# Performance work log

Measured on AMD Instinct MI355X. Metric: run time of the kernel, lower is better.

The kernel has to match this reference:

```python
import jax, jax.numpy as jnp
import numpy as np

NUM_TYPES = 8
NUM_TAGS = 1 + 2 * NUM_TYPES  # tag 0 = 'O', 2t+1 = 'B-t', 2t+2 = 'I-t'
NEG = -10000.0


def _bio_constraints(num_types):
    K = 1 + 2 * num_types
    allowed = np.zeros((K, K), dtype=np.float32)
    for i in range(K):
        for j in range(K):
            if j == 0 or (j % 2 == 1):  # to O or to B-y: always allowed
                allowed[i, j] = 1.0
            else:  # to I-y: only from B-y or I-y
                y = (j - 2) // 2
                if i in (2 * y + 1, 2 * y + 2):
                    allowed[i, j] = 1.0
    start = np.array([1.0 if (j == 0 or j % 2 == 1) else 0.0 for j in range(K)], dtype=np.float32)
    end = np.ones((K,), dtype=np.float32)  # BIO: any tag may end a sequence
    return allowed, start, end


def setup_inputs() -> dict:
    key = jax.random.key(0)
    ks = jax.random.split(key, 8)
    B, T, D, K = 64, 512, 1024, NUM_TAGS
    mlm_out = jax.random.normal(ks[0], (B, T, D), dtype=jnp.float32)
    lengths = jax.random.randint(ks[1], (B,), T // 4, T + 1)  # variable lengths >= 1
    mask = (jnp.arange(T)[None, :] < lengths[:, None])  # bool [B,T], left-padded-free
    gold = jax.random.randint(ks[2], (B, T), 0, K)
    W = jax.random.normal(ks[3], (D, K), dtype=jnp.float32) * 0.02
    b = jnp.zeros((K,), dtype=jnp.float32)
    transitions = jax.random.normal(ks[4], (K, K), dtype=jnp.float32) * 0.1
    start_trans = jax.random.normal(ks[5], (K,), dtype=jnp.float32) * 0.1
    end_trans = jax.random.normal(ks[6], (K,), dtype=jnp.float32) * 0.1
    ta, sa, ea = _bio_constraints(NUM_TYPES)
    return {"mlm_out": mlm_out, "mask": mask, "gold": gold, "W": W, "b": b,
            "transitions": transitions, "start_trans": start_trans, "end_trans": end_trans,
            "trans_allowed": jnp.asarray(ta), "start_allowed": jnp.asarray(sa), "end_allowed": jnp.asarray(ea)}


def reference(mlm_out, mask, gold, W, b, transitions, start_trans, end_trans,
              trans_allowed, start_allowed, end_allowed):
    logits = jnp.einsum('btd,dk->btk', mlm_out, W) + b  # [B,T,K]
    maskf = mask.astype(logits.dtype)
    B, T, K = logits.shape

    # ---- joint (numerator) score, AllenNLP semantics ----
    score = start_trans[gold[:, 0]]
    pair = transitions[gold[:, :-1], gold[:, 1:]]                       # [B,T-1]
    emit = jnp.take_along_axis(logits, gold[:, :, None], axis=2)[..., 0]  # [B,T]
    score = score + jnp.sum(pair * maskf[:, 1:], axis=1) + jnp.sum(emit[:, :-1] * maskf[:, :-1], axis=1)
    lengths = jnp.sum(mask.astype(jnp.int32), axis=1)
    last_tags = jnp.take_along_axis(gold, (lengths - 1)[:, None], axis=1)[:, 0]
    last_emit = jnp.take_along_axis(logits[:, -1, :], last_tags[:, None], axis=1)[:, 0]
    score = score + end_trans[last_tags] + last_emit * maskf[:, -1]

    # ---- partition function (forward algorithm, log-space scan over time) ----
    logits_t = jnp.swapaxes(logits, 0, 1)  # [T,B,K]
    mask_t = jnp.swapaxes(maskf, 0, 1)     # [T,B]
    alpha0 = start_trans + logits_t[0]

    def fstep(alpha, xs):
        emit_t, m = xs
        inner = alpha[:, :, None] + transitions[None] + emit_t[:, None, :]  # [B,K,K]
        new = jax.scipy.special.logsumexp(inner, axis=1)
        return jnp.where(m[:, None] > 0, new, alpha), None

    alphaT, _ = jax.lax.scan(fstep, alpha0, (logits_t[1:], mask_t[1:]))
    logZ = jax.scipy.special.logsumexp(alphaT + end_trans, axis=1)

    loss = -jnp.sum(score - logZ)  # loss_weight = 1.0

    # ---- Viterbi decode with BIO-constrained transitions ----
    ct = transitions * trans_allowed + NEG * (1.0 - trans_allowed)
    cs = start_trans * start_allowed + NEG * (1.0 - start_allowed)
    ce = end_trans * end_allowed + NEG * (1.0 - end_allowed)
    v0 = cs + logits_t[0]

    def vstep(v, xs):
        emit_t, m = xs
        inner = v[:, :, None] + ct[None]          # [B,K,K]
        bp = jnp.argmax(inner, axis=1)            # [B,K] best prev tag per next tag
        best = jnp.max(inner, axis=1) + emit_t
        return jnp.where(m[:, None] > 0, best, v), bp

    vT, bps = jax.lax.scan(vstep, v0, (logits_t[1:], mask_t[1:]))  # bps [T-1,B,K]
    last_tag = jnp.argmax(vT + ce, axis=1)  # [B]

    def btstep(tag, xs):
        bp, m = xs
        prev = jnp.take_along_axis(bp, tag[:, None], axis=1)[:, 0]
        prev = jnp.where(m > 0, prev, tag)  # padded steps: carry tag through
        return prev, tag

    first_tag, tags_rest = jax.lax.scan(btstep, last_tag, (bps, mask_t[1:]), reverse=True)
    pred = jnp.concatenate([first_tag[None], tags_rest], axis=0).swapaxes(0, 1)  # [B,T]
    pred = pred * mask.astype(pred.dtype)
    return logits, loss, pred
```

## Files before the change

### kernel.cpp

```cpp
#include <hip/hip_runtime.h>
#include <math.h>

#define KK 17
#define TT 512
#define DD 1024
#define NBATCH 64
#define NEGC -10000.0f
#define NINF -1e30f

__device__ __forceinline__ float wsum64(float v) {
#pragma unroll
  for (int s = 32; s >= 1; s >>= 1) v += __shfl_xor(v, s);
  return v;
}
__device__ __forceinline__ int wsum64i(int v) {
#pragma unroll
  for (int s = 32; s >= 1; s >>= 1) v += __shfl_xor(v, s);
  return v;
}
__device__ __forceinline__ float rl(float x, int i) {
  return __int_as_float(__builtin_amdgcn_readlane(__float_as_int(x), i));
}

__global__ __launch_bounds__(512) void k_logits(const float* __restrict__ X,
                                                const float* __restrict__ W,
                                                const float* __restrict__ b,
                                                float* __restrict__ logits) {
  __shared__ float Ws[512 * KK];
  const int tid = threadIdx.x;
  const int lane = tid & 63;
  const int wv = tid >> 6;
  const long r0 = (long)blockIdx.x * 16 + wv * 2;
  const float* x0 = X + r0 * DD;
  float a0[KK], a1[KK];
#pragma unroll
  for (int j = 0; j < KK; ++j) { a0[j] = 0.f; a1[j] = 0.f; }

  for (int half = 0; half < 2; ++half) {
    __syncthreads();
#pragma unroll
    for (int i = 0; i < KK; ++i) {
      int idx = tid + i * 512;
      Ws[idx] = W[half * 512 * KK + idx];
    }
    __syncthreads();
#pragma unroll
    for (int it = 0; it < 8; ++it) {
      int k = it * 64 + lane;
      float xa = x0[half * 512 + k];
      float xb = x0[DD + half * 512 + k];
#pragma unroll
      for (int j = 0; j < KK; ++j) {
        float w = Ws[k * KK + j];
        a0[j] = fmaf(xa, w, a0[j]);
        a1[j] = fmaf(xb, w, a1[j]);
      }
    }
  }
#pragma unroll
  for (int j = 0; j < KK; ++j) { a0[j] = wsum64(a0[j]); a1[j] = wsum64(a1[j]); }
  if (lane < KK) {
    float v0 = 0.f, v1 = 0.f;
#pragma unroll
    for (int j = 0; j < KK; ++j)
      if (lane == j) { v0 = a0[j]; v1 = a1[j]; }
    float bb = b[lane];
    logits[r0 * KK + lane] = v0 + bb;
    logits[(r0 + 1) * KK + lane] = v1 + bb;
  }
}

#define ARGM(vl, il, vr, ir, vo, io) \
  { bool tk = (vr) > (vl); vo = tk ? (vr) : (vl); io = tk ? (ir) : (il); }

__global__ __launch_bounds__(256) void k_scan(
    const float* __restrict__ logits, const void* __restrict__ maskp,
    const int* __restrict__ gold, const float* __restrict__ trans,
    const float* __restrict__ st, const float* __restrict__ et,
    const float* __restrict__ ta, const float* __restrict__ sa,
    const float* __restrict__ ea, float* __restrict__ lossp,
    float* __restrict__ predp) {
  __shared__ __align__(16) float EM[513 * KK];
  __shared__ __align__(4) unsigned char Mk[512];
  __shared__ unsigned char BPt[511 * KK];
  __shared__ unsigned char G2t[256 * KK];
  __shared__ unsigned char G4t[128 * KK];
  __shared__ unsigned char G8t[64 * KK];
  __shared__ unsigned char PR[512];
  __shared__ float red[2];
  __shared__ int shlt;

  const int tid = threadIdx.x;
  const int lane = tid & 63;
  const int wv = tid >> 6;
  const int batch = blockIdx.x;
  const float* Lg = logits + (size_t)batch * TT * KK;

  const unsigned char* mb = (const unsigned char*)maskp;
  const bool m_is_i32 = (mb[1] == 0);

  {
    const float4* Lg4 = reinterpret_cast<const float4*>(Lg);
    float4* EM4 = reinterpret_cast<float4*>(EM);
    for (int i = tid; i < (TT * KK) / 4; i += 256) EM4[i] = Lg4[i];
    if (m_is_i32) {
      const int* mi = (const int*)maskp + batch * TT;
      for (int t2 = tid; t2 < TT; t2 += 256) Mk[t2] = (unsigned char)(mi[t2] != 0);
    } else {
      const unsigned char* mB = mb + batch * TT;
      for (int t2 = tid; t2 < TT; t2 += 256) Mk[t2] = (unsigned char)(mB[t2] != 0);
    }
  }
  __syncthreads();
  int len;
  {
    const unsigned int* Mku = reinterpret_cast<const unsigned int*>(Mk);
    unsigned int a = Mku[lane], b2 = Mku[64 + lane];
    int c = (int)(((a * 0x01010101u) >> 24) + ((b2 * 0x01010101u) >> 24));
    len = wsum64i(c);
  }

  const int jc = lane < KK ? lane : (KK - 1);

  if (wv == 0) {
    float ctv[KK];
#pragma unroll
    for (int i = 0; i < KK; ++i)
      ctv[i] = (ta[i * KK + jc] > 0.5f) ? trans[i * KK + jc] : NEGC;
    float v = ((sa[jc] > 0.5f) ? st[jc] : NEGC) + EM[jc];
    float ec = EM[KK + jc];
    const float* EMp = EM + 2 * KK + jc;
    unsigned char* bpw = BPt + jc;
    const bool act = lane < KK;
    for (int t = 1; t < len; ++t) {
      float en = *EMp;
      EMp += KK;
      float c0 = rl(v, 0) + ctv[0],  c1 = rl(v, 1) + ctv[1];
      float c2 = rl(v, 2) + ctv[2],  c3 = rl(v, 3) + ctv[3];
      float c4 = rl(v, 4) + ctv[4],  c5 = rl(v, 5) + ctv[5];
      float c6 = rl(v, 6) + ctv[6],  c7 = rl(v, 7) + ctv[7];
      float c8 = rl(v, 8) + ctv[8],  c9 = rl(v, 9) + ctv[9];
      float c10 = rl(v, 10) + ctv[10], c11 = rl(v, 11) + ctv[11];
      float c12 = rl(v, 12) + ctv[12], c13 = rl(v, 13) + ctv[13];
      float c14 = rl(v, 14) + ctv[14], c15 = rl(v, 15) + ctv[15];
      float c16 = rl(v, 16) + ctv[16];
      float d0, d1, d2, d3, d4, d5, d6, d7;
      int j0, j1, j2, j3, j4, j5, j6, j7;
      ARGM(c0, 0, c1, 1, d0, j0)     ARGM(c2, 2, c3, 3, d1, j1)
      ARGM(c4, 4, c5, 5, d2, j2)     ARGM(c6, 6, c7, 7, d3, j3)
      ARGM(c8, 8, c9, 9, d4, j4)     ARGM(c10, 10, c11, 11, d5, j5)
      ARGM(c12, 12, c13, 13, d6, j6) ARGM(c14, 14, c15, 15, d7, j7)
      float e0, e1, e2, e3; int k0, k1, k2, k3;
      ARGM(d0, j0, d1, j1, e0, k0)   ARGM(d2, j2, d3, j3, e1, k1)
      ARGM(d4, j4, d5, j5, e2, k2)   ARGM(d6, j6, d7, j7, e3, k3)
      float f0, f1; int l0, l1;
      ARGM(e0, k0, e1, k1, f0, l0)   ARGM(e2, k2, e3, k3, f1, l1)
      float g0; int m0i;
      ARGM(f0, l0, f1, l1, g0, m0i)
      float bv; int bi;
      ARGM(g0, m0i, c16, 16, bv, bi)
      if (act) bpw[0] = (unsigned char)bi;
      bpw += KK;
      v = bv + ec;
      ec = en;
    }
    float fv = v + ((ea[jc] > 0.5f) ? et[jc] : NEGC);
    float best = rl(fv, 0);
    int bidx = 0;
#pragma unroll
    for (int i = 1; i < KK; ++i) {
      float fi = rl(fv, i);
      bool tk = fi > best;
      best = tk ? fi : best;
      bidx = tk ? i : bidx;
    }
    if (tid == 0) shlt = bidx;
  } else if (wv == 1) {
    float Pcol[KK];
#pragma unroll
    for (int i = 0; i < KK; ++i) Pcol[i] = __expf(trans[i * KK + jc]);
    float a0 = st[jc] + EM[jc];
    float m0 = rl(a0, 0);
#pragma unroll
    for (int i = 1; i < KK; ++i) m0 = fmaxf(m0, rl(a0, i));
    float qown = __expf(a0 - m0);
    float C = m0;
    float ee = __expf(EM[KK + jc]);
    const float* EMp = EM + 2 * KK + jc;
    for (int t = 1; t < len; ++t) {
      float en_raw = *EMp;
      EMp += KK;
      float q0 = rl(qown, 0), q1 = rl(qown, 1), q2 = rl(qown, 2), q3 = rl(qown, 3);
      float q4 = rl(qown, 4), q5 = rl(qown, 5), q6 = rl(qown, 6), q7 = rl(qown, 7);
      float q8 = rl(qown, 8), q9 = rl(qown, 9), q10 = rl(qown, 10), q11 = rl(qown, 11);
      float q12 = rl(qown, 12), q13 = rl(qown, 13), q14 = rl(qown, 14), q15 = rl(qown, 15);
      float q16 = rl(qown, 16);
      float da = fmaf(q0, Pcol[0], fmaf(q4, Pcol[4], fmaf(q8, Pcol[8], fmaf(q12, Pcol[12], q16 * Pcol[16]))));
      float db = fmaf(q1, Pcol[1], fmaf(q5, Pcol[5], fmaf(q9, Pcol[9], q13 * Pcol[13])));
      float dc = fmaf(q2, Pcol[2], fmaf(q6, Pcol[6], fmaf(q10, Pcol[10], q14 * Pcol[14])));
      float dd = fmaf(q3, Pcol[3], fmaf(q7, Pcol[7], fmaf(q11, Pcol[11], q15 * Pcol[15])));
      float qn = ((da + db) + (dc + dd)) * ee;
      ee = __expf(en_raw);
      if ((t & 7) == 0) {
        float s0 = ((q0 + q1) + (q2 + q3)) + ((q4 + q5) + (q6 + q7));
        float s1 = ((q8 + q9) + (q10 + q11)) + ((q12 + q13) + (q14 + q15));
        float s = (s0 + s1) + q16;
        C += __logf(s);
        qn *= (1.0f / s);
      }
      qown = qn;
    }
    float term = qown * __expf(et[jc]);
    float S = rl(term, 0);
#pragma unroll
    for (int i = 1; i < KK; ++i) S += rl(term, i);
    if (lane == 0) red[0] = C + __logf(S);
  } else if (wv == 2) {
    const int* gb = gold + batch * TT;
    float esum = 0.f, tsum = 0.f;
#pragma unroll
    for (int u = 0; u < 8; ++u) {
      int t = lane + 64 * u;
      int gt = gb[t];
      float mt = (float)Mk[t];
      esum += mt * EM[t * KK + gt];
      int tn = (t + 1 < TT) ? t + 1 : TT - 1;
      int gn = gb[tn];
      float mtr = (t + 1 < TT && Mk[t + 1]) ? 1.f : 0.f;
      tsum += mtr * trans[gt * KK + gn];
    }
    float ssum = wsum64(esum + tsum);
    if (lane == 0) red[1] = ssum + st[gb[0]] + et[gb[len - 1]];
  }
  __syncthreads();
  if (tid == 0) atomicAdd(lossp, red[0] - red[1]);

  const int lt = shlt;
  {
    int m = tid;
    int s1 = 2 * m + 1, s0b = 2 * m;
    bool u1 = (s1 < 511) && Mk[s1 + 1];
    bool u0 = Mk[s0b + 1] != 0;
#pragma unroll
    for (int x = 0; x < KK; ++x) {
      int y = u1 ? (int)BPt[s1 * KK + x] : x;
      int z = u0 ? (int)BPt[s0b * KK + y] : y;
      G2t[m * KK + x] = (unsigned char)z;
    }
  }
  __syncthreads();
  if (tid < 128) {
    int p = tid;
#pragma unroll
    for (int x = 0; x < KK; ++x) {
      int y = G2t[(2 * p + 1) * KK + x];
      G4t[p * KK + x] = G2t[2 * p * KK + y];
    }
  }
  __syncthreads();
  if (tid < 64) {
    int p = tid;
#pragma unroll
    for (int x = 0; x < KK; ++x) {
      int y = G4t[(2 * p + 1) * KK + x];
      G8t[p * KK + x] = G4t[2 * p * KK + y];
    }
  }
  __syncthreads();
  if (tid == 0) {
    int x = lt;
    for (int p = 63; p >= 0; --p) {
      x = G8t[p * KK + x];
      PR[8 * p] = (unsigned char)x;
    }
  }
  __syncthreads();
  if (tid < 64) {
    int p = tid;
    int src = (p == 63) ? lt : (int)PR[8 * p + 8];
    PR[8 * p + 4] = G4t[(2 * p + 1) * KK + src];
  }
  __syncthreads();
  if (tid < 128) {
    int m = tid;
    int src = (m == 127) ? lt : (int)PR[4 * m + 4];
    PR[4 * m + 2] = G2t[(2 * m + 1) * KK + src];
  }
  __syncthreads();
  {
    int m = tid;
    int s = 2 * m + 1;
    int src = (m == 255) ? lt : (int)PR[2 * m + 2];
    int val = ((s < 511) && Mk[s + 1]) ? (int)BPt[s * KK + src] : src;
    PR[2 * m + 1] = (unsigned char)val;
  }
  __syncthreads();
  float* po = predp + batch * TT;
  for (int t2 = tid; t2 < TT; t2 += 256) po[t2] = Mk[t2] ? (float)PR[t2] : 0.f;
}

extern "C" void kernel_launch(void* const* d_in, const int* in_sizes, int n_in,
                              void* d_out, int out_size, void* d_ws, size_t ws_size,
                              hipStream_t stream) {
  const float* mlm = (const float*)d_in[0];
  const void* mask = d_in[1];
  const int* gold = (const int*)d_in[2];
  const float* W = (const float*)d_in[3];
  const float* b = (const float*)d_in[4];
  const float* trans = (const float*)d_in[5];
  const float* st = (const float*)d_in[6];
  const float* et = (const float*)d_in[7];
  const float* ta = (const float*)d_in[8];
  const float* sa = (const float*)d_in[9];
  const float* ea = (const float*)d_in[10];

  float* out = (float*)d_out;
  float* logits = out;
  float* lossp = out + (size_t)NBATCH * TT * KK;
  float* predp = lossp + 1;

  hipMemsetAsync(lossp, 0, sizeof(float), stream);
  k_logits<<<dim3(2048), dim3(512), 0, stream>>>(mlm, W, b, logits);
  k_scan<<<dim3(64), dim3(256), 0, stream>>>(logits, mask, gold, trans, st, et,
                                             ta, sa, ea, lossp, predp);
}
```

Baseline: 368.3 us.

## Process four rows per wave in logits GEMV and transpose emissions for fixed-trip scans

The logits kernel now computes four rows per wave instead of two, so each shared-memory W load is reused across more rows, and it launches half as many blocks. The scan kernel stores emissions transposed per tag so each lane can fetch four timesteps with one float4 load. The Viterbi and forward recurrences become fully unrolled fixed-length loops that select on t<len instead of exiting at len. This removes per-step LDS loads and loop overhead, but every batch now runs all 511 steps regardless of its length, and the GEMV uses more registers.

```diff
diff --git a/kernel.cpp b/kernel.cpp
--- a/kernel.cpp
+++ b/kernel.cpp
@@ -7,6 +7,7 @@
 #define NBATCH 64
 #define NEGC -10000.0f
 #define NINF -1e30f
+#define EMS 516
 
 __device__ __forceinline__ float wsum64(float v) {
 #pragma unroll
@@ -30,11 +31,11 @@
   const int tid = threadIdx.x;
   const int lane = tid & 63;
   const int wv = tid >> 6;
-  const long r0 = (long)blockIdx.x * 16 + wv * 2;
+  const long r0 = (long)blockIdx.x * 32 + wv * 4;
   const float* x0 = X + r0 * DD;
-  float a0[KK], a1[KK];
-#pragma unroll
-  for (int j = 0; j < KK; ++j) { a0[j] = 0.f; a1[j] = 0.f; }
+  float a0[KK], a1[KK], a2[KK], a3[KK];
+#pragma unroll
+  for (int j = 0; j < KK; ++j) { a0[j] = 0.f; a1[j] = 0.f; a2[j] = 0.f; a3[j] = 0.f; }
 
   for (int half = 0; half < 2; ++half) {
     __syncthreads();
@@ -49,24 +50,33 @@
       int k = it * 64 + lane;
       float xa = x0[half * 512 + k];
       float xb = x0[DD + half * 512 + k];
+      float xc = x0[2 * DD + half * 512 + k];
+      float xd = x0[3 * DD + half * 512 + k];
 #pragma unroll
       for (int j = 0; j < KK; ++j) {
         float w = Ws[k * KK + j];
         a0[j] = fmaf(xa, w, a0[j]);
         a1[j] = fmaf(xb, w, a1[j]);
+        a2[j] = fmaf(xc, w, a2[j]);
+        a3[j] = fmaf(xd, w, a3[j]);
       }
     }
   }
 #pragma unroll
-  for (int j = 0; j < KK; ++j) { a0[j] = wsum64(a0[j]); a1[j] = wsum64(a1[j]); }
+  for (int j = 0; j < KK; ++j) {
+    a0[j] = wsum64(a0[j]); a1[j] = wsum64(a1[j]);
+    a2[j] = wsum64(a2[j]); a3[j] = wsum64(a3[j]);
+  }
   if (lane < KK) {
-    float v0 = 0.f, v1 = 0.f;
+    float v0 = 0.f, v1 = 0.f, v2 = 0.f, v3 = 0.f;
 #pragma unroll
     for (int j = 0; j < KK; ++j)
-      if (lane == j) { v0 = a0[j]; v1 = a1[j]; }
+      if (lane == j) { v0 = a0[j]; v1 = a1[j]; v2 = a2[j]; v3 = a3[j]; }
     float bb = b[lane];
     logits[r0 * KK + lane] = v0 + bb;
     logits[(r0 + 1) * KK + lane] = v1 + bb;
+    logits[(r0 + 2) * KK + lane] = v2 + bb;
+    logits[(r0 + 3) * KK + lane] = v3 + bb;
   }
 }
 
@@ -80,7 +90,7 @@
     const float* __restrict__ ta, const float* __restrict__ sa,
     const float* __restrict__ ea, float* __restrict__ lossp,
     float* __restrict__ predp) {
-  __shared__ __align__(16) float EM[513 * KK];
+  __shared__ __align__(16) float EMT[KK * EMS];
   __shared__ __align__(4) unsigned char Mk[512];
   __shared__ unsigned char BPt[511 * KK];
   __shared__ unsigned char G2t[256 * KK];
@@ -101,8 +111,18 @@
 
   {
     const float4* Lg4 = reinterpret_cast<const float4*>(Lg);
-    float4* EM4 = reinterpret_cast<float4*>(EM);
-    for (int i = tid; i < (TT * KK) / 4; i += 256) EM4[i] = Lg4[i];
+    for (int i = tid; i < (TT * KK) / 4; i += 256) {
+      float4 v = Lg4[i];
+      int n = i * 4;
+      int t0 = n / KK, j0 = n - t0 * KK;
+      float vv[4] = {v.x, v.y, v.z, v.w};
+#pragma unroll
+      for (int e = 0; e < 4; ++e) {
+        int j = j0 + e, t = t0;
+        if (j >= KK) { j -= KK; t += 1; }
+        EMT[j * EMS + t] = vv[e];
+      }
+    }
     if (m_is_i32) {
       const int* mi = (const int*)maskp + batch * TT;
       for (int t2 = tid; t2 < TT; t2 += 256) Mk[t2] = (unsigned char)(mi[t2] != 0);
@@ -121,49 +141,60 @@
   }
 
   const int jc = lane < KK ? lane : (KK - 1);
+  const float* EMTrow = EMT + jc * EMS;
 
   if (wv == 0) {
     float ctv[KK];
 #pragma unroll
     for (int i = 0; i < KK; ++i)
       ctv[i] = (ta[i * KK + jc] > 0.5f) ? trans[i * KK + jc] : NEGC;
-    float v = ((sa[jc] > 0.5f) ? st[jc] : NEGC) + EM[jc];
-    float ec = EM[KK + jc];
-    const float* EMp = EM + 2 * KK + jc;
     unsigned char* bpw = BPt + jc;
     const bool act = lane < KK;
-    for (int t = 1; t < len; ++t) {
-      float en = *EMp;
-      EMp += KK;
-      float c0 = rl(v, 0) + ctv[0],  c1 = rl(v, 1) + ctv[1];
-      float c2 = rl(v, 2) + ctv[2],  c3 = rl(v, 3) + ctv[3];
-      float c4 = rl(v, 4) + ctv[4],  c5 = rl(v, 5) + ctv[5];
-      float c6 = rl(v, 6) + ctv[6],  c7 = rl(v, 7) + ctv[7];
-      float c8 = rl(v, 8) + ctv[8],  c9 = rl(v, 9) + ctv[9];
-      float c10 = rl(v, 10) + ctv[10], c11 = rl(v, 11) + ctv[11];
-      float c12 = rl(v, 12) + ctv[12], c13 = rl(v, 13) + ctv[13];
-      float c14 = rl(v, 14) + ctv[14], c15 = rl(v, 15) + ctv[15];
-      float c16 = rl(v, 16) + ctv[16];
-      float d0, d1, d2, d3, d4, d5, d6, d7;
-      int j0, j1, j2, j3, j4, j5, j6, j7;
-      ARGM(c0, 0, c1, 1, d0, j0)     ARGM(c2, 2, c3, 3, d1, j1)
-      ARGM(c4, 4, c5, 5, d2, j2)     ARGM(c6, 6, c7, 7, d3, j3)
-      ARGM(c8, 8, c9, 9, d4, j4)     ARGM(c10, 10, c11, 11, d5, j5)
-      ARGM(c12, 12, c13, 13, d6, j6) ARGM(c14, 14, c15, 15, d7, j7)
-      float e0, e1, e2, e3; int k0, k1, k2, k3;
-      ARGM(d0, j0, d1, j1, e0, k0)   ARGM(d2, j2, d3, j3, e1, k1)
-      ARGM(d4, j4, d5, j5, e2, k2)   ARGM(d6, j6, d7, j7, e3, k3)
-      float f0, f1; int l0, l1;
-      ARGM(e0, k0, e1, k1, f0, l0)   ARGM(e2, k2, e3, k3, f1, l1)
-      float g0; int m0i;
-      ARGM(f0, l0, f1, l1, g0, m0i)
-      float bv; int bi;
-      ARGM(g0, m0i, c16, 16, bv, bi)
-      if (act) bpw[0] = (unsigned char)bi;
-      bpw += KK;
-      v = bv + ec;
-      ec = en;
-    }
+    float4 A = *reinterpret_cast<const float4*>(EMTrow);
+    float v = ((sa[jc] > 0.5f) ? st[jc] : NEGC) + A.x;
+    int t = 1;
+
+#define VSTEP(EMV)                                                        \
+    {                                                                     \
+      float c0 = rl(v, 0) + ctv[0], c1 = rl(v, 1) + ctv[1];               \
+      float c2 = rl(v, 2) + ctv[2], c3 = rl(v, 3) + ctv[3];               \
+      float c4 = rl(v, 4) + ctv[4], c5 = rl(v, 5) + ctv[5];               \
+      float c6 = rl(v, 6) + ctv[6], c7 = rl(v, 7) + ctv[7];               \
+      float c8 = rl(v, 8) + ctv[8], c9 = rl(v, 9) + ctv[9];               \
+      float c10 = rl(v, 10) + ctv[10], c11 = rl(v, 11) + ctv[11];         \
+      float c12 = rl(v, 12) + ctv[12], c13 = rl(v, 13) + ctv[13];         \
+      float c14 = rl(v, 14) + ctv[14], c15 = rl(v, 15) + ctv[15];         \
+      float c16 = rl(v, 16) + ctv[16];                                    \
+      float d0, d1, d2, d3, d4, d5, d6, d7;                               \
+      int j0, j1, j2, j3, j4, j5, j6, j7;                                 \
+      ARGM(c0, 0, c1, 1, d0, j0) ARGM(c2, 2, c3, 3, d1, j1)               \
+      ARGM(c4, 4, c5, 5, d2, j2) ARGM(c6, 6, c7, 7, d3, j3)               \
+      ARGM(c8, 8, c9, 9, d4, j4) ARGM(c10, 10, c11, 11, d5, j5)           \
+      ARGM(c12, 12, c13, 13, d6, j6) ARGM(c14, 14, c15, 15, d7, j7)       \
+      float e0, e1, e2, e3; int k0, k1, k2, k3;                           \
+      ARGM(d0, j0, d1, j1, e0, k0) ARGM(d2, j2, d3, j3, e1, k1)           \
+      ARGM(d4, j4, d5, j5, e2, k2) ARGM(d6, j6, d7, j7, e3, k3)           \
+      float f0, f1; int l0, l1;                                           \
+      ARGM(e0, k0, e1, k1, f0, l0) ARGM(e2, k2, e3, k3, f1, l1)           \
+      float g0; int m0i;                                                  \
+      ARGM(f0, l0, f1, l1, g0, m0i)                                       \
+      float bv; int bi;                                                   \
+      ARGM(g0, m0i, c16, 16, bv, bi)                                      \
+      if (act) bpw[0] = (unsigned char)bi;                                \
+      bpw += KK;                                                          \
+      float vn = bv + (EMV);                                              \
+      v = (t < len) ? vn : v;                                             \
+      ++t;                                                                \
+    }
+
+    for (int g = 0; g < 127; ++g) {
+      float4 B = *reinterpret_cast<const float4*>(EMTrow + 4 * g + 4);
+      VSTEP(A.y) VSTEP(A.z) VSTEP(A.w) VSTEP(B.x)
+      A = B;
+    }
+    VSTEP(A.y) VSTEP(A.z) VSTEP(A.w)
+#undef VSTEP
+
     float fv = v + ((ea[jc] > 0.5f) ? et[jc] : NEGC);
     float best = rl(fv, 0);
     int bidx = 0;
@@ -179,37 +210,55 @@
     float Pcol[KK];
 #pragma unroll
     for (int i = 0; i < KK; ++i) Pcol[i] = __expf(trans[i * KK + jc]);
-    float a0 = st[jc] + EM[jc];
-    float m0 = rl(a0, 0);
-#pragma unroll
-    for (int i = 1; i < KK; ++i) m0 = fmaxf(m0, rl(a0, i));
-    float qown = __expf(a0 - m0);
+    float4 A = *reinterpret_cast<const float4*>(EMTrow);
+    float a0v = st[jc] + A.x;
+    float m0 = rl(a0v, 0);
+#pragma unroll
+    for (int i = 1; i < KK; ++i) m0 = fmaxf(m0, rl(a0v, i));
+    float qown = __expf(a0v - m0);
     float C = m0;
-    float ee = __expf(EM[KK + jc]);
-    const float* EMp = EM + 2 * KK + jc;
-    for (int t = 1; t < len; ++t) {
-      float en_raw = *EMp;
-      EMp += KK;
-      float q0 = rl(qown, 0), q1 = rl(qown, 1), q2 = rl(qown, 2), q3 = rl(qown, 3);
-      float q4 = rl(qown, 4), q5 = rl(qown, 5), q6 = rl(qown, 6), q7 = rl(qown, 7);
-      float q8 = rl(qown, 8), q9 = rl(qown, 9), q10 = rl(qown, 10), q11 = rl(qown, 11);
-      float q12 = rl(qown, 12), q13 = rl(qown, 13), q14 = rl(qown, 14), q15 = rl(qown, 15);
-      float q16 = rl(qown, 16);
-      float da = fmaf(q0, Pcol[0], fmaf(q4, Pcol[4], fmaf(q8, Pcol[8], fmaf(q12, Pcol[12], q16 * Pcol[16]))));
-      float db = fmaf(q1, Pcol[1], fmaf(q5, Pcol[5], fmaf(q9, Pcol[9], q13 * Pcol[13])));
-      float dc = fmaf(q2, Pcol[2], fmaf(q6, Pcol[6], fmaf(q10, Pcol[10], q14 * Pcol[14])));
-      float dd = fmaf(q3, Pcol[3], fmaf(q7, Pcol[7], fmaf(q11, Pcol[11], q15 * Pcol[15])));
-      float qn = ((da + db) + (dc + dd)) * ee;
-      ee = __expf(en_raw);
-      if ((t & 7) == 0) {
-        float s0 = ((q0 + q1) + (q2 + q3)) + ((q4 + q5) + (q6 + q7));
-        float s1 = ((q8 + q9) + (q10 + q11)) + ((q12 + q13) + (q14 + q15));
-        float s = (s0 + s1) + q16;
-        C += __logf(s);
-        qn *= (1.0f / s);
-      }
-      qown = qn;
-    }
+    float ee = __expf(A.y);
+    int t = 1;
+
+#define FSTEP(EMNEXT, DOREN)                                                   \
+    {                                                                          \
+      float q0 = rl(qown, 0), q1 = rl(qown, 1), q2 = rl(qown, 2);              \
+      float q3 = rl(qown, 3), q4 = rl(qown, 4), q5 = rl(qown, 5);              \
+      float q6 = rl(qown, 6), q7 = rl(qown, 7), q8 = rl(qown, 8);              \
+      float q9 = rl(qown, 9), q10 = rl(qown, 10), q11 = rl(qown, 11);          \
+      float q12 = rl(qown, 12), q13 = rl(qown, 13), q14 = rl(qown, 14);        \
+      float q15 = rl(qown, 15), q16 = rl(qown, 16);                            \
+      float da = fmaf(q0, Pcol[0], fmaf(q4, Pcol[4], fmaf(q8, Pcol[8],         \
+                 fmaf(q12, Pcol[12], q16 * Pcol[16]))));                       \
+      float db = fmaf(q1, Pcol[1], fmaf(q5, Pcol[5], fmaf(q9, Pcol[9],         \
+                 q13 * Pcol[13])));                                            \
+      float dc = fmaf(q2, Pcol[2], fmaf(q6, Pcol[6], fmaf(q10, Pcol[10],       \
+                 q14 * Pcol[14])));                                            \
+      float dd = fmaf(q3, Pcol[3], fmaf(q7, Pcol[7], fmaf(q11, Pcol[11],       \
+                 q15 * Pcol[15])));                                            \
+      float qn = ((da + db) + (dc + dd)) * ee;                                 \
+      ee = __expf(EMNEXT);                                                     \
+      float qs = (t < len) ? qn : qown;                                        \
+      if (DOREN) {                                                             \
+        float s0 = ((q0 + q1) + (q2 + q3)) + ((q4 + q5) + (q6 + q7));          \
+        float s1 = ((q8 + q9) + (q10 + q11)) + ((q12 + q13) + (q14 + q15));    \
+        float s = (s0 + s1) + q16;                                             \
+        C += __logf(s);                                                        \
+        qs *= (1.0f / s);                                                      \
+      }                                                                        \
+      qown = qs;                                                               \
+      ++t;                                                                     \
+    }
+
+    for (int g = 0; g < 127; ++g) {
+      float4 B = *reinterpret_cast<const float4*>(EMTrow + 4 * g + 4);
+      FSTEP(A.z, false) FSTEP(A.w, false) FSTEP(B.x, false)
+      FSTEP(B.y, (g & 1))
+      A = B;
+    }
+    FSTEP(A.z, false) FSTEP(A.w, false) FSTEP(A.w, false)
+#undef FSTEP
+
     float term = qown * __expf(et[jc]);
     float S = rl(term, 0);
 #pragma unroll
@@ -223,7 +272,7 @@
       int t = lane + 64 * u;
       int gt = gb[t];
       float mt = (float)Mk[t];
-      esum += mt * EM[t * KK + gt];
+      esum += mt * EMT[gt * EMS + t];
       int tn = (t + 1 < TT) ? t + 1 : TT - 1;
       int gn = gb[tn];
       float mtr = (t + 1 < TT && Mk[t + 1]) ? 1.f : 0.f;
@@ -320,7 +369,7 @@
   float* predp = lossp + 1;
 
   hipMemsetAsync(lossp, 0, sizeof(float), stream);
-  k_logits<<<dim3(2048), dim3(512), 0, stream>>>(mlm, W, b, logits);
+  k_logits<<<dim3(1024), dim3(512), 0, stream>>>(mlm, W, b, logits);
   k_scan<<<dim3(64), dim3(256), 0, stream>>>(logits, mask, gold, trans, st, et,
                                              ta, sa, ea, lossp, predp);
 }
```

Measured after the change: 375.7 us. 2.0% more time.
